# Kernel tuning notes

Measured on AMD Instinct MI355X. Metric: run time of the kernel, lower is better.

## Reference

```python
import jax, jax.numpy as jnp
import numpy as np

NUM_CLASSES = 2
THRESHOLD = 0.35   # overlap_thresh
NEG_POS = 7        # negative:positive mining ratio
VAR0, VAR1 = 0.1, 0.2  # self.variance


def point_form(boxes):
    # (cx,cy,w,h) -> (xmin,ymin,xmax,ymax); boxes [P,4]
    return jnp.concatenate([boxes[:, :2] - boxes[:, 2:] / 2,
                            boxes[:, :2] + boxes[:, 2:] / 2], axis=1)


def jaccard(box_a, box_b):
    # box_a [B,O,4] xyxy, box_b [P,4] xyxy -> IoU [B,O,P]
    max_xy = jnp.minimum(box_a[:, :, None, 2:], box_b[None, None, :, 2:])
    min_xy = jnp.maximum(box_a[:, :, None, :2], box_b[None, None, :, :2])
    wh = jnp.clip(max_xy - min_xy, 0.0)
    inter = wh[..., 0] * wh[..., 1]
    area_a = ((box_a[..., 2] - box_a[..., 0]) * (box_a[..., 3] - box_a[..., 1]))[:, :, None]
    area_b = ((box_b[:, 2] - box_b[:, 0]) * (box_b[:, 3] - box_b[:, 1]))[None, None, :]
    return inter / (area_a + area_b - inter)


def encode(matched, priors):
    # matched [B,P,4] xyxy, priors [1,P,4] cxcywh -> offsets [B,P,4]
    g_cxcy = (matched[..., :2] + matched[..., 2:]) / 2 - priors[..., :2]
    g_cxcy = g_cxcy / (VAR0 * priors[..., 2:])
    g_wh = (matched[..., 2:] - matched[..., :2]) / priors[..., 2:]
    g_wh = jnp.log(g_wh) / VAR1
    return jnp.concatenate([g_cxcy, g_wh], axis=-1)


def match(truths, labels, priors):
    # truths [B,O,4] xyxy, labels [B,O] float, priors [P,4] cxcywh
    overlaps = jaccard(truths, point_form(priors))      # [B,O,P]
    best_prior_idx = jnp.argmax(overlaps, axis=2)       # [B,O] best prior per gt
    best_truth_overlap = jnp.max(overlaps, axis=1)      # [B,P]
    best_truth_idx = jnp.argmax(overlaps, axis=1)       # [B,P] best gt per prior
    O = truths.shape[1]

    def fix(bto, bti, bpi):
        # ensure every gt keeps its best prior (index_fill_ / loop in torch)
        bto = bto.at[bpi].set(2.0)
        bti = bti.at[bpi].set(jnp.arange(O))
        return bto, bti

    best_truth_overlap, best_truth_idx = jax.vmap(fix)(
        best_truth_overlap, best_truth_idx, best_prior_idx)
    matched = jnp.take_along_axis(truths, best_truth_idx[..., None], axis=1)  # [B,P,4]
    conf = jnp.take_along_axis(labels, best_truth_idx, axis=1).astype(jnp.int32) + 1
    conf = jnp.where(best_truth_overlap < THRESHOLD, 0, conf)  # background
    loc = encode(matched, priors[None])
    return loc, conf


def setup_inputs() -> dict:
    key = jax.random.key(0)
    k1, k2, k3, k4, k5, k6 = jax.random.split(key, 6)
    B, P, O, C = 32, 32768, 32, NUM_CLASSES
    loc_data = jax.random.normal(k1, (B, P, 4), jnp.float32)
    conf_data = jax.random.normal(k2, (B, P, C), jnp.float32)
    # priors: (cx,cy,w,h) in [0,1], wh in [0.02,0.3]
    p_cxcy = jax.random.uniform(k3, (P, 2), jnp.float32)
    p_wh = 0.02 + 0.28 * jax.random.uniform(k4, (P, 2), jnp.float32)
    priors = jnp.concatenate([p_cxcy, p_wh], axis=1)
    # targets: valid xyxy boxes + label column (label 0 -> class 1 after +1)
    t_cxcy = 0.1 + 0.8 * jax.random.uniform(k5, (B, O, 2), jnp.float32)
    t_wh = 0.05 + 0.2 * jax.random.uniform(k6, (B, O, 2), jnp.float32)
    boxes = jnp.concatenate([t_cxcy - t_wh / 2, t_cxcy + t_wh / 2], axis=2)
    labels = jnp.zeros((B, O, 1), jnp.float32)
    targets = jnp.concatenate([boxes, labels], axis=2)
    return {"loc_data": loc_data, "conf_data": conf_data,
            "priors": priors, "targets": targets}


def reference(loc_data, conf_data, priors, targets):
    B, P, C = conf_data.shape
    truths = targets[..., :4]
    labels = targets[..., 4]
    loc_t, conf_t = match(truths, labels, priors)   # [B,P,4], [B,P] int
    pos = conf_t > 0                                # [B,P]

    # localization: smooth-L1 summed over positives
    diff = loc_data - loc_t
    ad = jnp.abs(diff)
    sl1 = jnp.where(ad < 1.0, 0.5 * diff * diff, ad - 0.5)
    loss_l = jnp.sum(sl1 * pos[..., None].astype(loc_data.dtype))

    # per-prior CE loss for hard-negative mining
    lse = jax.nn.logsumexp(conf_data, axis=2)                            # [B,P]
    picked = jnp.take_along_axis(conf_data, conf_t[..., None], axis=2)[..., 0]
    ce = lse - picked                                                    # [B,P]
    mine = jnp.where(pos, 0.0, ce)
    # double-argsort rank trick (descending)
    loss_idx = jnp.argsort(-mine, axis=1)
    idx_rank = jnp.argsort(loss_idx, axis=1)
    num_pos = jnp.sum(pos, axis=1, keepdims=True)                        # [B,1]
    num_neg = jnp.minimum(NEG_POS * num_pos, P - 1)
    neg = idx_rank < num_neg

    sel = pos | neg
    loss_c = jnp.sum(jnp.where(sel, ce, 0.0))

    N = jnp.maximum(jnp.sum(num_pos).astype(jnp.float32), 1.0)
    return loss_l / N, loss_c / N
```

## Files before the change

### kernel.cpp

```cpp
#include <hip/hip_runtime.h>
#include <stdint.h>

#define NB 32
#define NP 32768
#define NO 32
#define THRESH 0.35f

typedef unsigned long long u64;
typedef unsigned int u32;

__device__ __forceinline__ float iou_corners(float px1, float py1, float px2, float py2, float ab,
                                             float tx1, float ty1, float tx2, float ty2, float aa)
{
#pragma clang fp contract(off)
    float iw = fminf(tx2, px2) - fmaxf(tx1, px1);
    float ih = fminf(ty2, py2) - fmaxf(ty1, py1);
    iw = fmaxf(iw, 0.f); ih = fmaxf(ih, 0.f);
    float inter = iw * ih;
    return __fdividef(inter, aa + ab - inter);
}

__device__ __forceinline__ float smooth_l1_sum(float4 ld, float4 pr, float4 tt)
{
#pragma clang fp contract(off)
    float g0 = ((tt.x + tt.z) * 0.5f - pr.x) / (0.1f * pr.z);
    float g1 = ((tt.y + tt.w) * 0.5f - pr.y) / (0.1f * pr.w);
    float g2 = __logf((tt.z - tt.x) / pr.z) / 0.2f;
    float g3 = __logf((tt.w - tt.y) / pr.w) / 0.2f;
    float d0 = ld.x - g0, d1 = ld.y - g1, d2 = ld.z - g2, d3 = ld.w - g3;
    float a0 = fabsf(d0), a1 = fabsf(d1), a2 = fabsf(d2), a3 = fabsf(d3);
    return (a0 < 1.f ? 0.5f * d0 * d0 : a0 - 0.5f)
         + (a1 < 1.f ? 0.5f * d1 * d1 : a1 - 0.5f)
         + (a2 < 1.f ? 0.5f * d2 * d2 : a2 - 0.5f)
         + (a3 < 1.f ? 0.5f * d3 * d3 : a3 - 0.5f);
}

__device__ __forceinline__ float lse2(float c0, float c1)
{
#pragma clang fp contract(off)
    float mm = fmaxf(c0, c1), mn = fminf(c0, c1);
    return mm + __logf(1.f + __expf(mn - mm));
}

__global__ __launch_bounds__(256) void kern1(
        const float* __restrict__ loc, const float* __restrict__ conf,
        const float* __restrict__ priors, const float* __restrict__ targets,
        float* __restrict__ mine, u64* __restrict__ bpk_part,
        float* __restrict__ part_sl1, float* __restrict__ part_cep, int* __restrict__ part_np)
{
#pragma clang fp contract(off)
    __shared__ __align__(16) float4 tbc[NO];
    __shared__ float ta[NO], tlab[NO];
    __shared__ u64 keys[NO];
    __shared__ float rs0[4], rs1[4];
    __shared__ int rc[4];
    const int b = blockIdx.y, x = blockIdx.x, tid = threadIdx.x;
    if (tid < NO * 5) {
        int o = tid / 5, c = tid % 5;
        float v = targets[b * NO * 5 + tid];
        if (c < 4) ((float*)&tbc[o])[c] = v; else tlab[o] = v;
    }
    if (tid < NO) keys[tid] = 0ull;
    __syncthreads();
    if (tid < NO) {
        float4 t = tbc[tid];
        ta[tid] = (t.z - t.x) * (t.w - t.y);
    }
    __syncthreads();

    const int p0 = x * 1024 + tid * 4;
    float4 pr[4];
    float px1[4], py1[4], px2[4], py2[4], ab[4];
#pragma unroll
    for (int j = 0; j < 4; ++j) {
        pr[j] = ((const float4*)priors)[p0 + j];
        px1[j] = pr[j].x - pr[j].z * 0.5f;
        py1[j] = pr[j].y - pr[j].w * 0.5f;
        px2[j] = pr[j].x + pr[j].z * 0.5f;
        py2[j] = pr[j].y + pr[j].w * 0.5f;
        ab[j]  = pr[j].z * pr[j].w;
    }
    u64 bk[4] = {0ull, 0ull, 0ull, 0ull};
    const int lane_o = tid & 31;
    for (int it = 0; it < NO; ++it) {
        const int o = (it + lane_o) & 31;
        float4 tt = tbc[o];
        float aa = ta[o];
        float iou4[4];
#pragma unroll
        for (int j = 0; j < 4; ++j) {
            float iou = iou_corners(px1[j], py1[j], px2[j], py2[j], ab[j],
                                    tt.x, tt.y, tt.z, tt.w, aa);
            iou4[j] = iou;
            u64 ko = ((u64)__float_as_uint(iou) << 6) | (u64)(63 - o);
            bk[j] = bk[j] > ko ? bk[j] : ko;
        }
        float vm = fmaxf(fmaxf(iou4[0], iou4[1]), fmaxf(iou4[2], iou4[3]));
        u32 vb = __float_as_uint(vm);
        u64 cur = keys[o];
        if (vb > (u32)(cur >> 32)) {
            float bi = iou4[3]; int bp = p0 + 3;
            if (iou4[2] >= bi) { bi = iou4[2]; bp = p0 + 2; }
            if (iou4[1] >= bi) { bi = iou4[1]; bp = p0 + 1; }
            if (iou4[0] >= bi) { bi = iou4[0]; bp = p0 + 0; }
            atomicMax(&keys[o], ((u64)__float_as_uint(bi) << 32) | (u64)(~(u32)bp));
        }
    }

    const size_t gbase = (size_t)b * NP + p0;
    float4 cfa = ((const float4*)conf)[gbase / 2];
    float4 cfb = ((const float4*)conf)[gbase / 2 + 1];
    float c0[4] = {cfa.x, cfa.z, cfb.x, cfb.z};
    float c1[4] = {cfa.y, cfa.w, cfb.y, cfb.w};
    float4 mout;
    float s_sl1 = 0.f, s_cep = 0.f;
    int np = 0;
#pragma unroll
    for (int j = 0; j < 4; ++j) {
        u32 vb = (u32)(bk[j] >> 6);
        float bv = __uint_as_float(vb);
        int o = 63 - (int)(bk[j] & 63);
        int cf = (bv < THRESH) ? 0 : ((int)tlab[o] + 1);
        bool pos = cf > 0;
        float4 ld = ((const float4*)loc)[gbase + j];
        float sl1 = smooth_l1_sum(ld, pr[j], tbc[o]);
        float ce = lse2(c0[j], c1[j]) - ((cf == 0) ? c0[j] : c1[j]);
        if (pos) { s_sl1 += sl1; s_cep += ce; np++; }
        ((float*)&mout)[j] = pos ? 0.f : ce;
    }
    ((float4*)mine)[gbase / 4] = mout;

#pragma unroll
    for (int m = 32; m; m >>= 1) {
        s_sl1 += __shfl_xor(s_sl1, m, 64);
        s_cep += __shfl_xor(s_cep, m, 64);
        np    += __shfl_xor(np, m, 64);
    }
    int lane = tid & 63, w = tid >> 6;
    if (lane == 0) { rs0[w] = s_sl1; rs1[w] = s_cep; rc[w] = np; }
    __syncthreads();
    if (tid == 0) {
        float t0 = 0.f, t1 = 0.f; int t2 = 0;
        for (int i = 0; i < 4; ++i) { t0 += rs0[i]; t1 += rs1[i]; t2 += rc[i]; }
        part_sl1[b * 32 + x] = t0;
        part_cep[b * 32 + x] = t1;
        part_np [b * 32 + x] = t2;
    }
    if (tid < NO) bpk_part[(b * 32 + x) * 32 + tid] = keys[tid];
}

__global__ __launch_bounds__(1024) void kern3(
        const float* __restrict__ loc, const float* __restrict__ conf,
        const float* __restrict__ priors, const float* __restrict__ targets,
        const u64* __restrict__ bpk_part, const float* __restrict__ mine,
        const float* __restrict__ part_sl1, const float* __restrict__ part_cep,
        const int* __restrict__ part_np,
        float* __restrict__ bs, float* __restrict__ bc, int* __restrict__ bn)
{
#pragma clang fp contract(off)
    const int b = blockIdx.x, tid = threadIdx.x;
    __shared__ __align__(16) float4 tbc[NO];
    __shared__ float tlab[NO], tas[NO];
    __shared__ u32 pp[NO];
    __shared__ u32 flags[1024];
    __shared__ __align__(16) int h0[256];
    __shared__ __align__(16) int h1[4096];
    __shared__ __align__(16) int h2[4096];
    __shared__ u32 sh_prefix;
    __shared__ int sh_kk;
    __shared__ float sh_sl1, sh_cep;
    __shared__ int sh_np;
    __shared__ float rs[16];

    if (tid < NO * 5) {
        int o = tid / 5, c = tid % 5;
        float v = targets[b * NO * 5 + tid];
        if (c < 4) ((float*)&tbc[o])[c] = v; else tlab[o] = v;
    }
    flags[tid] = 0u;
    if (tid < 256) h0[tid] = 0;
    for (int i = tid; i < 4096; i += 1024) { h1[i] = 0; h2[i] = 0; }

    const float* mb = mine + (size_t)b * NP;
    float v[32];
#pragma unroll
    for (int q = 0; q < 8; ++q) {
        float4 t4 = ((const float4*)mb)[q * 1024 + tid];
        v[4 * q] = t4.x; v[4 * q + 1] = t4.y; v[4 * q + 2] = t4.z; v[4 * q + 3] = t4.w;
    }
    __syncthreads();
    if (tid < NO) {
        float4 t = tbc[tid];
        tas[tid] = (t.z - t.x) * (t.w - t.y);
        u64 key = 0ull;
        for (int xx = 0; xx < 32; ++xx) {
            u64 t2 = bpk_part[(b * 32 + xx) * 32 + tid];
            key = t2 > key ? t2 : key;
        }
        pp[tid] = (key >> 32) ? ~(u32)key : 0u;
    }
    __syncthreads();
    float dsl1 = 0.f, dcep = 0.f; int dnp = 0;
    if (tid < NO) {
        const int o = tid;
        const u32 p = pp[o];
        bool last = true;
        for (int o2 = o + 1; o2 < NO; ++o2)
            if (pp[o2] == p) { last = false; break; }
        if (last) {
            float4 prr = ((const float4*)priors)[p];
            float px1 = prr.x - prr.z * 0.5f, py1 = prr.y - prr.w * 0.5f;
            float px2 = prr.x + prr.z * 0.5f, py2 = prr.y + prr.w * 0.5f;
            float ab = prr.z * prr.w;
            float bv = -1.f; int bo_ = 0;
            for (int o2 = 0; o2 < NO; ++o2) {
                float4 t2 = tbc[o2];
                float i2 = iou_corners(px1, py1, px2, py2, ab, t2.x, t2.y, t2.z, t2.w, tas[o2]);
                if (i2 > bv) { bv = i2; bo_ = o2; }
            }
            int cf_pre = (bv < THRESH) ? 0 : ((int)tlab[bo_] + 1);
            size_t gp = (size_t)b * NP + p;
            float4 ld = ((const float4*)loc)[gp];
            float2 c = ((const float2*)conf)[gp];
            float lse = lse2(c.x, c.y);
            int cf_new = (int)tlab[o] + 1;
            dsl1 = smooth_l1_sum(ld, prr, tbc[o]);
            dcep = lse - ((cf_new == 0) ? c.x : c.y);
            dnp = 1;
            if (cf_pre > 0) {
                dsl1 -= smooth_l1_sum(ld, prr, tbc[bo_]);
                dcep -= lse - ((cf_pre == 0) ? c.x : c.y);
                dnp = 0;
            }
            atomicOr(&flags[p >> 5], 1u << (p & 31));
        }
        float a = part_sl1[b * 32 + o] + dsl1;
        float d = part_cep[b * 32 + o] + dcep;
        int   n = part_np [b * 32 + o] + dnp;
#pragma unroll
        for (int m = 16; m; m >>= 1) {
            a += __shfl_xor(a, m, 32);
            d += __shfl_xor(d, m, 32);
            n += __shfl_xor(n, m, 32);
        }
        if (o == 0) {
            sh_sl1 = a; sh_cep = d; sh_np = n;
            sh_prefix = 0u; sh_kk = min(7 * n, NP - 1);
        }
    }
    __syncthreads();
#pragma unroll
    for (int q = 0; q < 8; ++q) {
        u32 word = flags[q * 128 + (tid >> 3)];
#pragma unroll
        for (int c = 0; c < 4; ++c)
            if ((word >> (((tid & 7) << 2) + c)) & 1u) v[4 * q + c] = 0.f;
    }
    const int k = sh_kk;
    const int lane = tid & 63;
    float topk = 0.f;
    if (k > 0) {
#pragma unroll 4
        for (int j = 0; j < 32; ++j) {
            u32 bin = __float_as_uint(v[j]) >> 24;
            u64 todo = ~0ull;
            while (todo) {
                int leader = __ffsll((unsigned long long)todo) - 1;
                u32 lb = (u32)__shfl((int)bin, leader, 64);
                u64 mt = __ballot(bin == lb);
                if (lane == leader) atomicAdd(&h0[lb], (int)__popcll(mt));
                todo &= ~mt;
            }
        }
        __syncthreads();
        if (tid < 64) {
            int4 h4 = ((const int4*)h0)[tid];
            int s3 = h4.w, s2 = h4.z + s3, s1 = h4.y + s2, s0 = h4.x + s1;
            int acc = s0;
#pragma unroll
            for (int off = 1; off < 64; off <<= 1) {
                int u = __shfl_down(acc, off, 64);
                if (tid + off < 64) acc += u;
            }
            int excl = acc - s0;
            int kk = sh_kk;
            int cand = -1, nkk = 0;
            if (excl + s3 >= kk)      { cand = 4 * tid + 3; nkk = kk - excl; }
            else if (excl + s2 >= kk) { cand = 4 * tid + 2; nkk = kk - excl - s3; }
            else if (excl + s1 >= kk) { cand = 4 * tid + 1; nkk = kk - excl - s2; }
            else if (excl + s0 >= kk) { cand = 4 * tid + 0; nkk = kk - excl - s1; }
            int cmax = cand;
#pragma unroll
            for (int off = 1; off < 64; off <<= 1) cmax = max(cmax, __shfl_xor(cmax, off, 64));
            if (cand >= 0 && cand == cmax) { sh_prefix = (u32)cand; sh_kk = nkk; }
        }
        __syncthreads();
        {
            const u32 pfx = sh_prefix;
#pragma unroll 4
            for (int j = 0; j < 32; ++j) {
                u32 kb = __float_as_uint(v[j]);
                if ((kb >> 24) == pfx) atomicAdd(&h1[(kb >> 12) & 0xFFF], 1);
            }
            __syncthreads();
            if (tid < 64) {
                int tot = 0;
#pragma unroll
                for (int q = 0; q < 16; ++q) {
                    int4 xq = ((const int4*)h1)[tid * 16 + q];
                    tot += xq.x + xq.y + xq.z + xq.w;
                }
                int acc = tot;
#pragma unroll
                for (int off = 1; off < 64; off <<= 1) {
                    int u = __shfl_down(acc, off, 64);
                    if (tid + off < 64) acc += u;
                }
                int excl = acc - tot;
                int kk = sh_kk;
                if (excl < kk && excl + tot >= kk) {
                    int a2 = excl, sel = 0, nkk = 0; bool fnd = false;
                    for (int i = 63; i >= 0; --i) {
                        int cbin = h1[tid * 64 + i];
                        if (!fnd && a2 + cbin >= kk) { sel = i; nkk = kk - a2; fnd = true; }
                        a2 += cbin;
                    }
                    sh_prefix = (pfx << 12) | (u32)(tid * 64 + sel);
                    sh_kk = nkk;
                }
            }
            __syncthreads();
        }
        {
            const u32 pfx = sh_prefix;
#pragma unroll 4
            for (int j = 0; j < 32; ++j) {
                u32 kb = __float_as_uint(v[j]);
                if ((kb >> 12) == pfx) atomicAdd(&h2[kb & 0xFFF], 1);
            }
            __syncthreads();
            if (tid < 64) {
                int tot = 0;
#pragma unroll
                for (int q = 0; q < 16; ++q) {
                    int4 xq = ((const int4*)h2)[tid * 16 + q];
                    tot += xq.x + xq.y + xq.z + xq.w;
                }
                int acc = tot;
#pragma unroll
                for (int off = 1; off < 64; off <<= 1) {
                    int u = __shfl_down(acc, off, 64);
                    if (tid + off < 64) acc += u;
                }
                int excl = acc - tot;
                int kk = sh_kk;
                if (excl < kk && excl + tot >= kk) {
                    int a2 = excl, sel = 0, nkk = 0; bool fnd = false;
                    for (int i = 63; i >= 0; --i) {
                        int cbin = h2[tid * 64 + i];
                        if (!fnd && a2 + cbin >= kk) { sel = i; nkk = kk - a2; fnd = true; }
                        a2 += cbin;
                    }
                    sh_prefix = (pfx << 12) | (u32)(tid * 64 + sel);
                    sh_kk = nkk;
                }
            }
            __syncthreads();
        }
        const u32 T = sh_prefix;
        const float tval = __uint_as_float(T);
        float s = 0.f;
#pragma unroll
        for (int j = 0; j < 32; ++j)
            if (__float_as_uint(v[j]) > T) s += v[j];
#pragma unroll
        for (int m = 32; m; m >>= 1) s += __shfl_xor(s, m, 64);
        if (lane == 0) rs[tid >> 6] = s;
        __syncthreads();
        if (tid == 0) {
            float st = 0.f;
            for (int i = 0; i < 16; ++i) st += rs[i];
            topk = st + (float)sh_kk * tval;
        }
    }
    if (tid == 0) {
        bs[b] = sh_sl1;
        bc[b] = sh_cep + topk;
        bn[b] = sh_np;
    }
}

__global__ void kern4(const float* __restrict__ bs, const float* __restrict__ bc,
                      const int* __restrict__ bn, float* __restrict__ out)
{
    int tid = threadIdx.x;
    float s = (tid < NB) ? bs[tid] : 0.f;
    float c = (tid < NB) ? bc[tid] : 0.f;
    int   n = (tid < NB) ? bn[tid] : 0;
#pragma unroll
    for (int m = 32; m; m >>= 1) {
        s += __shfl_xor(s, m, 64);
        c += __shfl_xor(c, m, 64);
        n += __shfl_xor(n, m, 64);
    }
    if (tid == 0) {
        float N = fmaxf((float)n, 1.f);
        out[0] = s / N;
        out[1] = c / N;
    }
}

extern "C" void kernel_launch(void* const* d_in, const int* in_sizes, int n_in,
                              void* d_out, int out_size, void* d_ws, size_t ws_size,
                              hipStream_t stream) {
    const float* loc     = (const float*)d_in[0];
    const float* conf    = (const float*)d_in[1];
    const float* priors  = (const float*)d_in[2];
    const float* targets = (const float*)d_in[3];
    float* out = (float*)d_out;

    char* ws = (char*)d_ws;
    float* mine     = (float*)ws;
    u64*   bpk_part = (u64*)(ws + 4194304);
    float* part_sl1 = (float*)(ws + 4456448);
    float* part_cep = (float*)(ws + 4460544);
    int*   part_np  = (int*)(ws + 4464640);
    float* bs       = (float*)(ws + 4468736);
    float* bc       = (float*)(ws + 4468864);
    int*   bn       = (int*)(ws + 4468992);

    dim3 g1(32, NB);
    kern1<<<g1, 256, 0, stream>>>(loc, conf, priors, targets, mine, bpk_part,
                                  part_sl1, part_cep, part_np);
    kern3<<<NB, 1024, 0, stream>>>(loc, conf, priors, targets, bpk_part, mine,
                                   part_sl1, part_cep, part_np, bs, bc, bn);
    kern4<<<1, 64, 0, stream>>>(bs, bc, bn, out);
}
```

Before: 155.7 us.

## Replace radix select with per-wave 8-bit histograms and fuse final reduction

Rewrites the top-k threshold search in kern3 as four 8-bit radix passes over per-wave privatized shared histograms, replacing the earlier ballot-aggregated 8-bit pass followed by two 12-bit passes with serial bin scans. It also drops the kern4 launch by having the last kern3 block, found through an atomic done counter, write the final outputs. kern1 now zeroes the accumulators, divisions in the encode path become fast divides, and the rotated target iteration order is removed. This trades serial scans and a launch for more passes, float atomics whose order is non-deterministic, and possible LDS bank contention on atomicMax now that all lanes read the same target.

New measurement: 201.9 us. 1.3x slower.

```diff
diff --git a/kernel.cpp b/kernel.cpp
--- a/kernel.cpp
+++ b/kernel.cpp
@@ -23,10 +23,10 @@
 __device__ __forceinline__ float smooth_l1_sum(float4 ld, float4 pr, float4 tt)
 {
 #pragma clang fp contract(off)
-    float g0 = ((tt.x + tt.z) * 0.5f - pr.x) / (0.1f * pr.z);
-    float g1 = ((tt.y + tt.w) * 0.5f - pr.y) / (0.1f * pr.w);
-    float g2 = __logf((tt.z - tt.x) / pr.z) / 0.2f;
-    float g3 = __logf((tt.w - tt.y) / pr.w) / 0.2f;
+    float g0 = __fdividef((tt.x + tt.z) * 0.5f - pr.x, 0.1f * pr.z);
+    float g1 = __fdividef((tt.y + tt.w) * 0.5f - pr.y, 0.1f * pr.w);
+    float g2 = __logf(__fdividef(tt.z - tt.x, pr.z)) * 5.0f;
+    float g3 = __logf(__fdividef(tt.w - tt.y, pr.w)) * 5.0f;
     float d0 = ld.x - g0, d1 = ld.y - g1, d2 = ld.z - g2, d3 = ld.w - g3;
     float a0 = fabsf(d0), a1 = fabsf(d1), a2 = fabsf(d2), a3 = fabsf(d3);
     return (a0 < 1.f ? 0.5f * d0 * d0 : a0 - 0.5f)
@@ -46,7 +46,9 @@
         const float* __restrict__ loc, const float* __restrict__ conf,
         const float* __restrict__ priors, const float* __restrict__ targets,
         float* __restrict__ mine, u64* __restrict__ bpk_part,
-        float* __restrict__ part_sl1, float* __restrict__ part_cep, int* __restrict__ part_np)
+        float* __restrict__ part_sl1, float* __restrict__ part_cep, int* __restrict__ part_np,
+        float* __restrict__ sl_tot, float* __restrict__ c_tot,
+        int* __restrict__ np_tot, int* __restrict__ done_cnt)
 {
 #pragma clang fp contract(off)
     __shared__ __align__(16) float4 tbc[NO];
@@ -55,6 +57,9 @@
     __shared__ float rs0[4], rs1[4];
     __shared__ int rc[4];
     const int b = blockIdx.y, x = blockIdx.x, tid = threadIdx.x;
+    if (b == 0 && x == 0 && tid == 0) {
+        *sl_tot = 0.f; *c_tot = 0.f; *np_tot = 0; *done_cnt = 0;
+    }
     if (tid < NO * 5) {
         int o = tid / 5, c = tid % 5;
         float v = targets[b * NO * 5 + tid];
@@ -81,9 +86,7 @@
         ab[j]  = pr[j].z * pr[j].w;
     }
     u64 bk[4] = {0ull, 0ull, 0ull, 0ull};
-    const int lane_o = tid & 31;
-    for (int it = 0; it < NO; ++it) {
-        const int o = (it + lane_o) & 31;
+    for (int o = 0; o < NO; ++o) {
         float4 tt = tbc[o];
         float aa = ta[o];
         float iou4[4];
@@ -96,9 +99,8 @@
             bk[j] = bk[j] > ko ? bk[j] : ko;
         }
         float vm = fmaxf(fmaxf(iou4[0], iou4[1]), fmaxf(iou4[2], iou4[3]));
-        u32 vb = __float_as_uint(vm);
         u64 cur = keys[o];
-        if (vb > (u32)(cur >> 32)) {
+        if (__float_as_uint(vm) > (u32)(cur >> 32)) {
             float bi = iou4[3]; int bp = p0 + 3;
             if (iou4[2] >= bi) { bi = iou4[2]; bp = p0 + 2; }
             if (iou4[1] >= bi) { bi = iou4[1]; bp = p0 + 1; }
@@ -155,17 +157,19 @@
         const u64* __restrict__ bpk_part, const float* __restrict__ mine,
         const float* __restrict__ part_sl1, const float* __restrict__ part_cep,
         const int* __restrict__ part_np,
-        float* __restrict__ bs, float* __restrict__ bc, int* __restrict__ bn)
+        float* __restrict__ sl_tot, float* __restrict__ c_tot,
+        int* __restrict__ np_tot, int* __restrict__ done_cnt,
+        float* __restrict__ out)
 {
 #pragma clang fp contract(off)
     const int b = blockIdx.x, tid = threadIdx.x;
+    const int wave = tid >> 6, lane = tid & 63;
     __shared__ __align__(16) float4 tbc[NO];
     __shared__ float tlab[NO], tas[NO];
     __shared__ u32 pp[NO];
     __shared__ u32 flags[1024];
-    __shared__ __align__(16) int h0[256];
-    __shared__ __align__(16) int h1[4096];
-    __shared__ __align__(16) int h2[4096];
+    __shared__ __align__(16) int hist[16][256];
+    __shared__ __align__(16) int total[256];
     __shared__ u32 sh_prefix;
     __shared__ int sh_kk;
     __shared__ float sh_sl1, sh_cep;
@@ -178,8 +182,6 @@
         if (c < 4) ((float*)&tbc[o])[c] = v; else tlab[o] = v;
     }
     flags[tid] = 0u;
-    if (tid < 256) h0[tid] = 0;
-    for (int i = tid; i < 4096; i += 1024) { h1[i] = 0; h2[i] = 0; }
 
     const float* mb = mine + (size_t)b * NP;
     float v[32];
@@ -200,10 +202,10 @@
         pp[tid] = (key >> 32) ? ~(u32)key : 0u;
     }
     __syncthreads();
-    float dsl1 = 0.f, dcep = 0.f; int dnp = 0;
     if (tid < NO) {
         const int o = tid;
         const u32 p = pp[o];
+        float dsl1 = 0.f, dcep = 0.f; int dnp = 0;
         bool last = true;
         for (int o2 = o + 1; o2 < NO; ++o2)
             if (pp[o2] == p) { last = false; break; }
@@ -257,111 +259,50 @@
             if ((word >> (((tid & 7) << 2) + c)) & 1u) v[4 * q + c] = 0.f;
     }
     const int k = sh_kk;
-    const int lane = tid & 63;
     float topk = 0.f;
     if (k > 0) {
-#pragma unroll 4
-        for (int j = 0; j < 32; ++j) {
-            u32 bin = __float_as_uint(v[j]) >> 24;
-            u64 todo = ~0ull;
-            while (todo) {
-                int leader = __ffsll((unsigned long long)todo) - 1;
-                u32 lb = (u32)__shfl((int)bin, leader, 64);
-                u64 mt = __ballot(bin == lb);
-                if (lane == leader) atomicAdd(&h0[lb], (int)__popcll(mt));
-                todo &= ~mt;
-            }
-        }
-        __syncthreads();
-        if (tid < 64) {
-            int4 h4 = ((const int4*)h0)[tid];
-            int s3 = h4.w, s2 = h4.z + s3, s1 = h4.y + s2, s0 = h4.x + s1;
-            int acc = s0;
-#pragma unroll
-            for (int off = 1; off < 64; off <<= 1) {
-                int u = __shfl_down(acc, off, 64);
-                if (tid + off < 64) acc += u;
-            }
-            int excl = acc - s0;
-            int kk = sh_kk;
-            int cand = -1, nkk = 0;
-            if (excl + s3 >= kk)      { cand = 4 * tid + 3; nkk = kk - excl; }
-            else if (excl + s2 >= kk) { cand = 4 * tid + 2; nkk = kk - excl - s3; }
-            else if (excl + s1 >= kk) { cand = 4 * tid + 1; nkk = kk - excl - s2; }
-            else if (excl + s0 >= kk) { cand = 4 * tid + 0; nkk = kk - excl - s1; }
-            int cmax = cand;
-#pragma unroll
-            for (int off = 1; off < 64; off <<= 1) cmax = max(cmax, __shfl_xor(cmax, off, 64));
-            if (cand >= 0 && cand == cmax) { sh_prefix = (u32)cand; sh_kk = nkk; }
-        }
-        __syncthreads();
-        {
+        int* myh = &hist[wave][0];
+        for (int pass = 0; pass < 4; ++pass) {
+#pragma unroll
+            for (int i = 0; i < 4; ++i) ((int*)hist)[tid + i * 1024] = 0;
+            __syncthreads();
+            const int shift = 24 - 8 * pass;
             const u32 pfx = sh_prefix;
-#pragma unroll 4
+#pragma unroll 8
             for (int j = 0; j < 32; ++j) {
                 u32 kb = __float_as_uint(v[j]);
-                if ((kb >> 24) == pfx) atomicAdd(&h1[(kb >> 12) & 0xFFF], 1);
+                if ((u32)(((u64)kb) >> (shift + 8)) == pfx)
+                    atomicAdd(&myh[(kb >> shift) & 255], 1);
+            }
+            __syncthreads();
+            if (tid < 256) {
+                int s = 0;
+#pragma unroll
+                for (int w2 = 0; w2 < 16; ++w2) s += hist[w2][tid];
+                total[tid] = s;
             }
             __syncthreads();
             if (tid < 64) {
-                int tot = 0;
-#pragma unroll
-                for (int q = 0; q < 16; ++q) {
-                    int4 xq = ((const int4*)h1)[tid * 16 + q];
-                    tot += xq.x + xq.y + xq.z + xq.w;
-                }
-                int acc = tot;
+                int4 h4 = ((const int4*)total)[tid];
+                int s3 = h4.w, s2 = h4.z + s3, s1 = h4.y + s2, s0 = h4.x + s1;
+                int acc = s0;
 #pragma unroll
                 for (int off = 1; off < 64; off <<= 1) {
                     int u = __shfl_down(acc, off, 64);
                     if (tid + off < 64) acc += u;
                 }
-                int excl = acc - tot;
+                int excl = acc - s0;
                 int kk = sh_kk;
-                if (excl < kk && excl + tot >= kk) {
-                    int a2 = excl, sel = 0, nkk = 0; bool fnd = false;
-                    for (int i = 63; i >= 0; --i) {
-                        int cbin = h1[tid * 64 + i];
-                        if (!fnd && a2 + cbin >= kk) { sel = i; nkk = kk - a2; fnd = true; }
-                        a2 += cbin;
-                    }
-                    sh_prefix = (pfx << 12) | (u32)(tid * 64 + sel);
-                    sh_kk = nkk;
-                }
-            }
-            __syncthreads();
-        }
-        {
-            const u32 pfx = sh_prefix;
-#pragma unroll 4
-            for (int j = 0; j < 32; ++j) {
-                u32 kb = __float_as_uint(v[j]);
-                if ((kb >> 12) == pfx) atomicAdd(&h2[kb & 0xFFF], 1);
-            }
-            __syncthreads();
-            if (tid < 64) {
-                int tot = 0;
-#pragma unroll
-                for (int q = 0; q < 16; ++q) {
-                    int4 xq = ((const int4*)h2)[tid * 16 + q];
-                    tot += xq.x + xq.y + xq.z + xq.w;
-                }
-                int acc = tot;
-#pragma unroll
-                for (int off = 1; off < 64; off <<= 1) {
-                    int u = __shfl_down(acc, off, 64);
-                    if (tid + off < 64) acc += u;
-                }
-                int excl = acc - tot;
-                int kk = sh_kk;
-                if (excl < kk && excl + tot >= kk) {
-                    int a2 = excl, sel = 0, nkk = 0; bool fnd = false;
-                    for (int i = 63; i >= 0; --i) {
-                        int cbin = h2[tid * 64 + i];
-                        if (!fnd && a2 + cbin >= kk) { sel = i; nkk = kk - a2; fnd = true; }
-                        a2 += cbin;
-                    }
-                    sh_prefix = (pfx << 12) | (u32)(tid * 64 + sel);
+                int cand = -1, nkk = 0;
+                if (excl + s3 >= kk)      { cand = 4 * tid + 3; nkk = kk - excl; }
+                else if (excl + s2 >= kk) { cand = 4 * tid + 2; nkk = kk - excl - s3; }
+                else if (excl + s1 >= kk) { cand = 4 * tid + 1; nkk = kk - excl - s2; }
+                else if (excl + s0 >= kk) { cand = 4 * tid + 0; nkk = kk - excl - s1; }
+                int cmax = cand;
+#pragma unroll
+                for (int off = 1; off < 64; off <<= 1) cmax = max(cmax, __shfl_xor(cmax, off, 64));
+                if (cand >= 0 && cand == cmax) {
+                    sh_prefix = (pfx << 8) | (u32)(cand & 255);
                     sh_kk = nkk;
                 }
             }
@@ -375,7 +316,7 @@
             if (__float_as_uint(v[j]) > T) s += v[j];
 #pragma unroll
         for (int m = 32; m; m >>= 1) s += __shfl_xor(s, m, 64);
-        if (lane == 0) rs[tid >> 6] = s;
+        if (lane == 0) rs[wave] = s;
         __syncthreads();
         if (tid == 0) {
             float st = 0.f;
@@ -384,29 +325,19 @@
         }
     }
     if (tid == 0) {
-        bs[b] = sh_sl1;
-        bc[b] = sh_cep + topk;
-        bn[b] = sh_np;
-    }
-}
-
-__global__ void kern4(const float* __restrict__ bs, const float* __restrict__ bc,
-                      const int* __restrict__ bn, float* __restrict__ out)
-{
-    int tid = threadIdx.x;
-    float s = (tid < NB) ? bs[tid] : 0.f;
-    float c = (tid < NB) ? bc[tid] : 0.f;
-    int   n = (tid < NB) ? bn[tid] : 0;
-#pragma unroll
-    for (int m = 32; m; m >>= 1) {
-        s += __shfl_xor(s, m, 64);
-        c += __shfl_xor(c, m, 64);
-        n += __shfl_xor(n, m, 64);
-    }
-    if (tid == 0) {
-        float N = fmaxf((float)n, 1.f);
-        out[0] = s / N;
-        out[1] = c / N;
+        atomicAdd(sl_tot, sh_sl1);
+        atomicAdd(c_tot, sh_cep + topk);
+        atomicAdd(np_tot, sh_np);
+        __threadfence();
+        int d = atomicAdd(done_cnt, 1);
+        if (d == NB - 1) {
+            float sl = atomicAdd(sl_tot, 0.f);
+            float cc = atomicAdd(c_tot, 0.f);
+            int   np = atomicAdd(np_tot, 0);
+            float N = fmaxf((float)np, 1.f);
+            out[0] = sl / N;
+            out[1] = cc / N;
+        }
     }
 }
 
@@ -425,14 +356,16 @@
     float* part_sl1 = (float*)(ws + 4456448);
     float* part_cep = (float*)(ws + 4460544);
     int*   part_np  = (int*)(ws + 4464640);
-    float* bs       = (float*)(ws + 4468736);
-    float* bc       = (float*)(ws + 4468864);
-    int*   bn       = (int*)(ws + 4468992);
+    float* sl_tot   = (float*)(ws + 4468736);
+    float* c_tot    = (float*)(ws + 4468740);
+    int*   np_tot   = (int*)(ws + 4468744);
+    int*   done_cnt = (int*)(ws + 4468748);
 
     dim3 g1(32, NB);
     kern1<<<g1, 256, 0, stream>>>(loc, conf, priors, targets, mine, bpk_part,
-                                  part_sl1, part_cep, part_np);
+                                  part_sl1, part_cep, part_np,
+                                  sl_tot, c_tot, np_tot, done_cnt);
     kern3<<<NB, 1024, 0, stream>>>(loc, conf, priors, targets, bpk_part, mine,
-                                   part_sl1, part_cep, part_np, bs, bc, bn);
-    kern4<<<1, 64, 0, stream>>>(bs, bc, bn, out);
-}
+                                   part_sl1, part_cep, part_np,
+                                   sl_tot, c_tot, np_tot, done_cnt, out);
+}
```
